# Optimization experiments

Hardware: AMD Instinct MI355X
Metric: run time of the kernel (lower is better)

## Reference

```python
import jax, jax.numpy as jnp
import numpy as np

F_DIM = 128
EDGE_DIM = 41
N_CONV = 6
N_GRAPHS = 128
EPS = 1e-5


def _bn(h, g, b, m, v):
    # eval-mode BatchNorm1d with running stats
    return (h - m) * (g / jnp.sqrt(v + EPS)) + b


def setup_inputs() -> dict:
    key = jax.random.key(0)
    ks = jax.random.split(key, 40)
    N, E = 20000, 320000
    inp = {}
    inp['x'] = jax.random.normal(ks[0], (N, 98), dtype=jnp.float32)
    inp['edge_index'] = jax.random.randint(ks[1], (2, E), 0, N, dtype=jnp.int32)
    inp['edge_attr'] = jax.random.uniform(ks[2], (E, EDGE_DIM), dtype=jnp.float32)
    inp['batch'] = jnp.sort(jax.random.randint(ks[3], (N,), 0, N_GRAPHS, dtype=jnp.int32))
    s = 0.05
    inp['embed_W'] = jax.random.normal(ks[4], (98, F_DIM), dtype=jnp.float32) * s
    inp['embed_b'] = jnp.zeros((F_DIM,), jnp.float32)
    Z = 2 * F_DIM + EDGE_DIM  # 297
    inp['conv_Wf'] = jax.random.normal(ks[5], (N_CONV, Z, F_DIM), dtype=jnp.float32) * s
    inp['conv_bf'] = jnp.zeros((N_CONV, F_DIM), jnp.float32)
    inp['conv_Ws'] = jax.random.normal(ks[6], (N_CONV, Z, F_DIM), dtype=jnp.float32) * s
    inp['conv_bs'] = jnp.zeros((N_CONV, F_DIM), jnp.float32)
    # inner (CGConv) BN params + running stats
    inp['bn_in_g'] = jnp.ones((N_CONV, F_DIM), jnp.float32)
    inp['bn_in_b'] = jnp.zeros((N_CONV, F_DIM), jnp.float32)
    inp['bn_in_m'] = jax.random.normal(ks[7], (N_CONV, F_DIM), dtype=jnp.float32) * 0.1
    inp['bn_in_v'] = jax.random.uniform(ks[8], (N_CONV, F_DIM), dtype=jnp.float32) + 0.5
    # outer BN params + running stats
    inp['bn_out_g'] = jnp.ones((N_CONV, F_DIM), jnp.float32)
    inp['bn_out_b'] = jnp.zeros((N_CONV, F_DIM), jnp.float32)
    inp['bn_out_m'] = jax.random.normal(ks[9], (N_CONV, F_DIM), dtype=jnp.float32) * 0.1
    inp['bn_out_v'] = jax.random.uniform(ks[10], (N_CONV, F_DIM), dtype=jnp.float32) + 0.5
    inp['pool_W'] = jax.random.normal(ks[11], (2 * F_DIM, F_DIM), dtype=jnp.float32) * s
    inp['pool_b'] = jnp.zeros((F_DIM,), jnp.float32)
    inp['f1_W'] = jax.random.normal(ks[12], (F_DIM, 256), dtype=jnp.float32) * s
    inp['f1_b'] = jnp.zeros((256,), jnp.float32)
    inp['f2_W'] = jax.random.normal(ks[13], (256, 128), dtype=jnp.float32) * s
    inp['f2_b'] = jnp.zeros((128,), jnp.float32)
    inp['f3_W'] = jax.random.normal(ks[14], (128, 1), dtype=jnp.float32) * s
    inp['f3_b'] = jnp.zeros((1,), jnp.float32)
    inp['d1_W'] = jax.random.normal(ks[15], (F_DIM, 256), dtype=jnp.float32) * s
    inp['d1_b'] = jnp.zeros((256,), jnp.float32)
    inp['d2_W'] = jax.random.normal(ks[16], (256, 384), dtype=jnp.float32) * s
    inp['d2_b'] = jnp.zeros((384,), jnp.float32)
    return inp


def reference(x, edge_index, edge_attr, batch,
              embed_W, embed_b,
              conv_Wf, conv_bf, conv_Ws, conv_bs,
              bn_in_g, bn_in_b, bn_in_m, bn_in_v,
              bn_out_g, bn_out_b, bn_out_m, bn_out_v,
              pool_W, pool_b,
              f1_W, f1_b, f2_W, f2_b, f3_W, f3_b,
              d1_W, d1_b, d2_W, d2_b):
    N = x.shape[0]
    src, dst = edge_index[0], edge_index[1]  # PyG: messages flow src(j) -> dst(i)
    h = x @ embed_W + embed_b  # [N, F]
    for i in range(N_CONV):
        h_res = h
        # CGConv: z = [x_i, x_j, e_ij]; m = sigmoid(lin_f(z)) * softplus(lin_s(z))
        z = jnp.concatenate([h[dst], h[src], edge_attr], axis=-1)  # [E, 297]
        m = jax.nn.sigmoid(z @ conv_Wf[i] + conv_bf[i]) * jax.nn.softplus(z @ conv_Ws[i] + conv_bs[i])
        agg = jax.ops.segment_sum(m, dst, num_segments=N)  # scatter-add to target nodes
        agg = _bn(agg, bn_in_g[i], bn_in_b[i], bn_in_m[i], bn_in_v[i])  # CGConv internal BN
        h = agg + h  # CGConv residual
        h = _bn(h, bn_out_g[i], bn_out_b[i], bn_out_m[i], bn_out_v[i])  # outer BN
        if i > 0:
            h = h + h_res
        # dropout: identity in eval mode
    # global mean / max pool by graph id
    sums = jax.ops.segment_sum(h, batch, num_segments=N_GRAPHS)
    counts = jax.ops.segment_sum(jnp.ones((N,), h.dtype), batch, num_segments=N_GRAPHS)
    x_mean = sums / jnp.maximum(counts, 1.0)[:, None]
    x_max = jax.ops.segment_max(h, batch, num_segments=N_GRAPHS)
    x_max = jnp.where(jnp.isfinite(x_max), x_max, 0.0)
    x_pool = jnp.concatenate([x_mean, x_max], axis=-1)  # [B, 2F]
    emb = jax.nn.relu(x_pool @ pool_W + pool_b)  # [B, F]
    f = jax.nn.silu(emb @ f1_W + f1_b)
    f = jax.nn.silu(f @ f2_W + f2_b)
    formation = f @ f3_W + f3_b  # [B, 1]
    d = jax.nn.silu(emb @ d1_W + d1_b)
    dos = (d @ d2_W + d2_b).reshape(-1, 3, 128)  # [B, 3, 128]
    return formation, dos
```

## Files before the change

kernel.cpp:

```cpp
#include <hip/hip_runtime.h>
#include <hip/hip_bf16.h>
#include <math.h>

typedef __attribute__((ext_vector_type(8))) _Float16 half8;
typedef __attribute__((ext_vector_type(4))) _Float16 half4;
typedef __attribute__((ext_vector_type(4))) float f32x4;
typedef __attribute__((ext_vector_type(4))) unsigned int u32x4;

#define FDIM 128
#define EPSBN 1e-5f
#define HSCALE_INV 0.015625f
#define WSCALE 64.0f
#define LOG2E 1.4426950408889634f
#define LN2   0.6931471805599453f

__global__ void prep_wn2(const float* __restrict__ Wf, const float* __restrict__ Ws,
                         _Float16* __restrict__ Wn2) {
    int idx = blockIdx.x * 256 + threadIdx.x;
    const int total = 6 * 65536;
    if (idx >= total) return;
    int j = idx & 7;
    int l15 = (idx >> 3) & 15;
    int lhi = (idx >> 7) & 3;
    int cb = (idx >> 9) & 31;
    int c4 = (idx >> 14) & 3;
    int i = idx >> 16;
    int col512 = cb * 16 + l15;
    int which = col512 >> 8;
    int colc = col512 & 255;
    int p = (colc >> 4) & 1;
    int f = ((colc >> 5) << 4) | (colc & 15);
    int k = c4 * 32 + lhi * 8 + j;
    int row = which * 128 + k;
    size_t o = ((size_t)i * 297 + row) * 128 + f;
    Wn2[idx] = (_Float16)((p ? Ws[o] : Wf[o]) * (WSCALE * LOG2E));
}

__global__ void prep_wb2(const float* __restrict__ Wf, const float* __restrict__ Ws,
                         _Float16* __restrict__ Wb2) {
    int idx = blockIdx.x * 256 + threadIdx.x;
    const int total = 6 * 16384;
    if (idx >= total) return;
    int j = idx & 7;
    int l15 = (idx >> 3) & 15;
    int lhi = (idx >> 7) & 3;
    int cb = (idx >> 9) & 15;
    int c2 = (idx >> 13) & 1;
    int i = idx >> 14;
    int k = c2 * 32 + lhi * 8 + j;
    int colc = cb * 16 + l15;
    int p = (colc >> 4) & 1;
    int f = ((colc >> 5) << 4) | (colc & 15);
    float v = 0.0f;
    if (k < 41) {
        size_t o = ((size_t)i * 297 + 256 + k) * 128 + f;
        v = (p ? Ws[o] : Wf[o]) * LOG2E;
    }
    Wb2[idx] = (_Float16)v;
}

__global__ void prep_we(const float* __restrict__ embW, _Float16* __restrict__ We) {
    int idx = blockIdx.x * 256 + threadIdx.x;
    if (idx >= 16384) return;
    int j = idx & 7;
    int l15 = (idx >> 3) & 15;
    int lhi = (idx >> 7) & 3;
    int cb = (idx >> 9) & 7;
    int c4 = (idx >> 12) & 3;
    int k = c4 * 32 + lhi * 8 + j;
    int f = cb * 16 + l15;
    We[idx] = (_Float16)((k < 98) ? embW[k * 128 + f] : 0.0f);
}

__global__ void prep_ht(const float* __restrict__ pW, const float* __restrict__ f1W,
                        const float* __restrict__ f2W, const float* __restrict__ d1W,
                        const float* __restrict__ d2W, float* __restrict__ HT) {
    int idx = blockIdx.x * 256 + threadIdx.x;
    if (idx < 32768) {
        int o = idx >> 8, k = idx & 255;
        HT[o * 256 + k] = pW[k * 128 + o];
    } else if (idx < 65536) {
        int r = idx - 32768; int o = r >> 7, k = r & 127;
        HT[32768 + o * 128 + k] = f1W[k * 256 + o];
    } else if (idx < 98304) {
        int r = idx - 65536; int o = r >> 8, k = r & 255;
        HT[65536 + o * 256 + k] = f2W[k * 128 + o];
    } else if (idx < 131072) {
        int r = idx - 98304; int o = r >> 7, k = r & 127;
        HT[98304 + o * 128 + k] = d1W[k * 256 + o];
    } else if (idx < 229376) {
        int r = idx - 131072; int o = r >> 8, k = r & 255;
        HT[131072 + o * 256 + k] = d2W[k * 384 + o];
    }
}

__global__ void prep_bn(const float* __restrict__ bing, const float* __restrict__ binb,
                        const float* __restrict__ binm, const float* __restrict__ binv,
                        const float* __restrict__ bog, const float* __restrict__ bob,
                        const float* __restrict__ bom, const float* __restrict__ bov,
                        float* __restrict__ ABC) {
    int idx = blockIdx.x * 128 + threadIdx.x;
    if (idx >= 6 * 128) return;
    int f = idx & 127;
    int i = idx >> 7;
    int o = i * 128 + f;
    float gin_ = bing[o] / sqrtf(binv[o] + EPSBN);
    float gout_ = bog[o] / sqrtf(bov[o] + EPSBN);
    ABC[i * 384 + f] = gin_ * gout_ * LN2;
    ABC[i * 384 + 128 + f] = gout_ + ((i > 0) ? 1.0f : 0.0f);
    ABC[i * 384 + 256 + f] = (binb[o] - binm[o] * gin_ - bom[o]) * gout_ + bob[o];
}

__global__ void hist_k(const int* __restrict__ dstI, int* __restrict__ cnt, int E) {
    int e = blockIdx.x * 256 + threadIdx.x;
    if (e < E) atomicAdd(&cnt[dstI[e]], 1);
}

__global__ void scan_k(const int* __restrict__ cnt, int* __restrict__ cursor, int N) {
    __shared__ int part[256];
    int t = threadIdx.x;
    int chunk = (N + 255) / 256;
    int lo = t * chunk, hi = lo + chunk; if (hi > N) hi = N;
    int s = 0;
    for (int i = lo; i < hi; ++i) s += cnt[i];
    part[t] = s;
    __syncthreads();
    for (int d = 1; d < 256; d <<= 1) {
        int v = (t >= d) ? part[t - d] : 0;
        __syncthreads();
        part[t] += v;
        __syncthreads();
    }
    int run = (t > 0) ? part[t - 1] : 0;
    for (int i = lo; i < hi; ++i) { cursor[i] = run; run += cnt[i]; }
}

__global__ void scatter_k(const int* __restrict__ srcI, const int* __restrict__ dstI,
                          int* __restrict__ cursor, unsigned* __restrict__ sdS,
                          int* __restrict__ invE, int E) {
    int e = blockIdx.x * 256 + threadIdx.x;
    if (e >= E) return;
    int d = dstI[e];
    int pos = atomicAdd(&cursor[d], 1);
    sdS[pos] = (unsigned)srcI[e] | ((unsigned)d << 16);
    invE[e] = pos;
}

__global__ void permute_ea2(const float* __restrict__ ea, const int* __restrict__ invE,
                            _Float16* __restrict__ eaH, int E) {
    int e = blockIdx.x * 4 + (threadIdx.x >> 6);
    int c = threadIdx.x & 63;
    if (e >= E) return;
    float v = (c < 41) ? ea[(size_t)e * 41 + c] : 0.0f;
    int pos = invE[e];
    eaH[(size_t)pos * 64 + c] = (_Float16)v;
}

__global__ __launch_bounds__(256, 4)
void embed_mm(const float* __restrict__ x, const _Float16* __restrict__ We,
              const float* __restrict__ b, float* __restrict__ h, int N) {
    __shared__ __align__(16) _Float16 xt[32 * 128];
    const int tid = threadIdx.x;
    const int nb = blockIdx.x * 32;

    {
        int e = tid >> 3, t = tid & 7;
        int node = nb + e; if (node >= N) node = N - 1;
        const float* row = x + (size_t)node * 98;
        __align__(16) _Float16 tmp[16];
        #pragma unroll
        for (int u = 0; u < 16; ++u) {
            int c = t * 16 + u;
            tmp[u] = (c < 98) ? (_Float16)row[c] : (_Float16)0.f;
        }
        int swz = (e & 7) << 4;
        *(u32x4*)((char*)xt + e * 256 + (((2 * t) * 16) ^ swz)) = *(u32x4*)tmp;
        *(u32x4*)((char*)xt + e * 256 + (((2 * t + 1) * 16) ^ swz)) = *(u32x4*)(tmp + 8);
    }
    __syncthreads();

    const int wid = tid >> 6;
    const int lane = tid & 63;
    const int l15 = lane & 15;
    const int lhi = lane >> 4;
    const int swzA = (l15 & 7) << 4;

    f32x4 acc[2][2];
    #pragma unroll
    for (int m = 0; m < 2; ++m)
        #pragma unroll
        for (int n = 0; n < 2; ++n) acc[m][n] = (f32x4){0.f, 0.f, 0.f, 0.f};

    #pragma unroll
    for (int c4 = 0; c4 < 4; ++c4) {
        half8 a[2];
        #pragma unroll
        for (int m = 0; m < 2; ++m) {
            int r = m * 16 + l15;
            a[m] = *(const half8*)((const char*)xt + r * 256 + ((c4 * 64 + lhi * 16) ^ swzA));
        }
        #pragma unroll
        for (int n = 0; n < 2; ++n) {
            int cb = wid * 2 + n;
            const half8 bf = *(const half8*)(We + ((((size_t)c4 * 8 + cb) * 4 + lhi) * 16 + l15) * 8);
            #pragma unroll
            for (int m = 0; m < 2; ++m)
                acc[m][n] = __builtin_amdgcn_mfma_f32_16x16x32_f16(a[m], bf, acc[m][n], 0, 0, 0);
        }
    }

    #pragma unroll
    for (int m = 0; m < 2; ++m) {
        #pragma unroll
        for (int n = 0; n < 2; ++n) {
            int feat = wid * 32 + n * 16 + l15;
            float bias = b[feat];
            #pragma unroll
            for (int j = 0; j < 4; ++j) {
                int node = nb + m * 16 + lhi * 4 + j;
                if (node < N) h[(size_t)node * 128 + feat] = acc[m][n][j] + bias;
            }
        }
    }
}

__global__ __launch_bounds__(256, 4)
void node_gemm_f(float* __restrict__ h, float* __restrict__ agg,
                 const _Float16* __restrict__ WnL, const float* __restrict__ ABC,
                 float* __restrict__ Pd4, float* __restrict__ Ps4, int N, int doBN) {
    __shared__ __align__(16) _Float16 ht[32 * 128];
    const int tid = threadIdx.x;
    const int nb = blockIdx.x * 32;

    {
        int e = tid >> 3, t = tid & 7;
        int node = nb + e; bool ok = (node < N); if (!ok) node = N - 1;
        const int c0 = t * 16;
        float* hrow = h + (size_t)node * 128 + c0;
        __align__(16) _Float16 tmp[16];
        if (doBN && ok) {
            float* arow = agg + (size_t)node * 128 + c0;
            #pragma unroll
            for (int u = 0; u < 16; u += 4) {
                f32x4 av = *(const f32x4*)(arow + u);
                f32x4 hv = *(const f32x4*)(hrow + u);
                f32x4 Av = *(const f32x4*)(ABC + c0 + u);
                f32x4 Bv = *(const f32x4*)(ABC + 128 + c0 + u);
                f32x4 Cv = *(const f32x4*)(ABC + 256 + c0 + u);
                f32x4 xv;
                #pragma unroll
                for (int j = 0; j < 4; ++j)
                    xv[j] = fmaf(av[j], Av[j], fmaf(hv[j], Bv[j], Cv[j]));
                *(f32x4*)(hrow + u) = xv;
                *(f32x4*)(arow + u) = (f32x4){0.f, 0.f, 0.f, 0.f};
                #pragma unroll
                for (int j = 0; j < 4; ++j) tmp[u + j] = (_Float16)(xv[j] * HSCALE_INV);
            }
        } else {
            #pragma unroll
            for (int u = 0; u < 16; u += 4) {
                f32x4 hv = *(const f32x4*)(hrow + u);
                #pragma unroll
                for (int j = 0; j < 4; ++j) tmp[u + j] = (_Float16)(hv[j] * HSCALE_INV);
            }
        }
        int swz = (e & 7) << 4;
        *(u32x4*)((char*)ht + e * 256 + (((2 * t) * 16) ^ swz)) = *(u32x4*)tmp;
        *(u32x4*)((char*)ht + e * 256 + (((2 * t + 1) * 16) ^ swz)) = *(u32x4*)(tmp + 8);
    }
    __syncthreads();

    f32x4 acc[2][8];
    #pragma unroll
    for (int m = 0; m < 2; ++m)
        #pragma unroll
        for (int n = 0; n < 8; ++n) acc[m][n] = (f32x4){0.f, 0.f, 0.f, 0.f};

    const int wid = tid >> 6;
    const int lane = tid & 63;
    const int l15 = lane & 15;
    const int lhi = lane >> 4;
    const int swzA = (l15 & 7) << 4;

    #pragma unroll
    for (int c4 = 0; c4 < 4; ++c4) {
        half8 a[2];
        #pragma unroll
        for (int m = 0; m < 2; ++m) {
            int r = m * 16 + l15;
            a[m] = *(const half8*)((const char*)ht + r * 256 + ((c4 * 64 + lhi * 16) ^ swzA));
        }
        #pragma unroll
        for (int n = 0; n < 8; ++n) {
            int cb = wid * 8 + n;
            const half8 bf = *(const half8*)(WnL +
                             ((((size_t)c4 * 32 + cb) * 4 + lhi) * 16 + l15) * 8);
            #pragma unroll
            for (int m = 0; m < 2; ++m)
                acc[m][n] = __builtin_amdgcn_mfma_f32_16x16x32_f16(a[m], bf, acc[m][n], 0, 0, 0);
        }
    }

    float* base = (wid < 2) ? Pd4 : Ps4;
    const int gw = (wid & 1) * 2;
    #pragma unroll
    for (int m = 0; m < 2; ++m) {
        #pragma unroll
        for (int j = 0; j < 4; ++j) {
            int node = nb + m * 16 + lhi * 4 + j;
            if (node < N) {
                #pragma unroll
                for (int nn = 0; nn < 2; ++nn) {
                    f32x4 v = { acc[m][4 * nn + 0][j], acc[m][4 * nn + 1][j],
                                acc[m][4 * nn + 2][j], acc[m][4 * nn + 3][j] };
                    *(f32x4*)(base + (size_t)node * 256 + ((gw + nn) * 16 + l15) * 4) = v;
                }
            }
        }
    }
}

__global__ __launch_bounds__(256, 4)
void edge_v11(const _Float16* __restrict__ eaH,
              const unsigned* __restrict__ sdS,
              const _Float16* __restrict__ WbL,
              const float* __restrict__ Pd4, const float* __restrict__ Ps4,
              const float* __restrict__ biasF, const float* __restrict__ biasS,
              float* __restrict__ agg) {
    __shared__ __align__(16) _Float16 eacc[64 * 256];
    __shared__ int srcl[64], dstl[64];

    const int tid = threadIdx.x;
    const int nblk = (int)gridDim.x;
    int lb = blockIdx.x;
    if ((nblk & 7) == 0) {
        int q = nblk >> 3;
        lb = (lb & 7) * q + (lb >> 3);
    }
    const int eb = lb * 64;

    if (tid < 64) {
        unsigned sd = sdS[eb + tid];
        srcl[tid] = (int)(sd & 0xFFFFu);
        dstl[tid] = (int)(sd >> 16);
    }

    const int wid = tid >> 6;
    const int lane = tid & 63;
    const int l15 = lane & 15;
    const int lhi = lane >> 4;

    f32x4 acc[4][4];
    #pragma unroll
    for (int m = 0; m < 4; ++m)
        #pragma unroll
        for (int n = 0; n < 4; ++n) acc[m][n] = (f32x4){0.f, 0.f, 0.f, 0.f};

    #pragma unroll
    for (int c2 = 0; c2 < 2; ++c2) {
        half8 a[4];
        #pragma unroll
        for (int m = 0; m < 4; ++m) {
            int r = m * 16 + l15;
            a[m] = *(const half8*)(eaH + (size_t)(eb + r) * 64 + c2 * 32 + lhi * 8);
        }
        #pragma unroll
        for (int n = 0; n < 4; ++n) {
            int cb = wid * 4 + n;
            const half8 b = *(const half8*)(WbL +
                            ((((size_t)c2 * 16 + cb) * 4 + lhi) * 16 + l15) * 8);
            #pragma unroll
            for (int m = 0; m < 4; ++m)
                acc[m][n] = __builtin_amdgcn_mfma_f32_16x16x32_f16(a[m], b, acc[m][n], 0, 0, 0);
        }
    }

    {
        const int g = (wid << 4) | l15;
        #pragma unroll
        for (int m = 0; m < 4; ++m) {
            #pragma unroll
            for (int j = 0; j < 4; ++j) {
                int r = m * 16 + lhi * 4 + j;
                half4 hv;
                hv[0] = (_Float16)acc[m][0][j];
                hv[1] = (_Float16)acc[m][1][j];
                hv[2] = (_Float16)acc[m][2][j];
                hv[3] = (_Float16)acc[m][3][j];
                *(half4*)(eacc + r * 256 + g * 4) = hv;
            }
        }
    }
    __syncthreads();

    const int f0 = ((lane >> 4) << 5) | l15;
    f32x4 b4;
    b4[0] = biasF[f0] * LOG2E;
    b4[1] = biasS[f0] * LOG2E;
    b4[2] = biasF[f0 + 16] * LOG2E;
    b4[3] = biasS[f0 + 16] * LOG2E;
    const int rbase = wid * 16;

    float s0 = 0.f, s1 = 0.f;
    int prevd = dstl[rbase];
    f32x4 pdb = *(const f32x4*)(Pd4 + (size_t)prevd * 256 + lane * 4);
    pdb += b4;

    f32x4 psq[4];
    #pragma unroll
    for (int e = 0; e < 4; ++e)
        psq[e] = *(const f32x4*)(Ps4 + (size_t)srcl[rbase + e] * 256 + lane * 4);

    #pragma unroll
    for (int e = 0; e < 16; ++e) {
        int r = rbase + e;
        int d = dstl[r];
        if (d != prevd) {
            pdb = *(const f32x4*)(Pd4 + (size_t)d * 256 + lane * 4);
            pdb += b4;
            prevd = d;
        }
        f32x4 psv = psq[e & 3];
        if (e + 4 < 16)
            psq[e & 3] = *(const f32x4*)(Ps4 + (size_t)srcl[r + 4] * 256 + lane * 4);
        half4 ev = *(const half4*)(eacc + r * 256 + lane * 4);
        float fp0 = (float)ev[0] + pdb[0] + psv[0];
        float sp0 = (float)ev[1] + pdb[1] + psv[1];
        float fp1 = (float)ev[2] + pdb[2] + psv[2];
        float sp1 = (float)ev[3] + pdb[3] + psv[3];
        float sig0 = __builtin_amdgcn_rcpf(1.0f + exp2f(-fp0));
        float spl0 = fmaxf(sp0, 0.0f) + __log2f(1.0f + exp2f(-fabsf(sp0)));
        float sig1 = __builtin_amdgcn_rcpf(1.0f + exp2f(-fp1));
        float spl1 = fmaxf(sp1, 0.0f) + __log2f(1.0f + exp2f(-fabsf(sp1)));
        s0 += sig0 * spl0;
        s1 += sig1 * spl1;
        bool flush = (e == 15) || (dstl[r + 1] != d);
        if (flush) {
            atomicAdd(&agg[(size_t)d * 128 + f0], s0);
            atomicAdd(&agg[(size_t)d * 128 + f0 + 16], s1);
            s0 = 0.f; s1 = 0.f;
        }
    }
}

__global__ void bn_final(const float* __restrict__ agg, float* __restrict__ h,
                         const float* __restrict__ ABC, int n128) {
    int idx = blockIdx.x * 256 + threadIdx.x;
    if (idx >= n128) return;
    int f = idx & 127;
    h[idx] = fmaf(agg[idx], ABC[f], fmaf(h[idx], ABC[128 + f], ABC[256 + f]));
}

__global__ __launch_bounds__(256, 4)
void pool2_k(const float* __restrict__ h, const int* __restrict__ batch,
             float* __restrict__ sums, unsigned* __restrict__ maxs,
             float* __restrict__ counts, int N) {
    const int f = threadIdx.x & 127;
    const int half = threadIdx.x >> 7;
    const int nb = blockIdx.x * 64 + half * 32;
    if (nb >= N) return;

    float s = 0.f;
    float mx = -3.4e38f;
    int prevg = -1;
    int runlen = 0;

    for (int e = 0; e < 32; ++e) {
        int n = nb + e;
        if (n >= N) break;
        int g = batch[n];
        if (g != prevg) {
            if (prevg >= 0) {
                atomicAdd(&sums[prevg * 128 + f], s);
                unsigned u = __float_as_uint(mx);
                unsigned key = (u & 0x80000000u) ? ~u : (u | 0x80000000u);
                atomicMax(&maxs[prevg * 128 + f], key);
                if (f == 0) atomicAdd(&counts[prevg], (float)runlen);
            }
            s = 0.f; mx = -3.4e38f; runlen = 0; prevg = g;
        }
        float v = h[(size_t)n * 128 + f];
        s += v;
        mx = fmaxf(mx, v);
        ++runlen;
    }
    if (prevg >= 0) {
        atomicAdd(&sums[prevg * 128 + f], s);
        unsigned u = __float_as_uint(mx);
        unsigned key = (u & 0x80000000u) ? ~u : (u | 0x80000000u);
        atomicMax(&maxs[prevg * 128 + f], key);
        if (f == 0) atomicAdd(&counts[prevg], (float)runlen);
    }
}

__global__ __launch_bounds__(256)
void head_k2(const float* __restrict__ sums, const unsigned* __restrict__ maxs,
             const float* __restrict__ counts, const float* __restrict__ HT,
             const float* __restrict__ pb, const float* __restrict__ f1b,
             const float* __restrict__ f2b, const float* __restrict__ f3W,
             const float* __restrict__ f3b, const float* __restrict__ d1b,
             const float* __restrict__ d2b, float* __restrict__ out) {
    __shared__ float xp[256], emb[128], s1[256], s2[128], dd[256];
    int g = blockIdx.x, t = threadIdx.x;
    float cnt = counts[g];
    if (t < 128) {
        float mean = sums[g * 128 + t] / fmaxf(cnt, 1.0f);
        float mx = 0.0f;
        if (cnt > 0.0f) {
            unsigned key = maxs[g * 128 + t];
            unsigned u = (key & 0x80000000u) ? (key & 0x7fffffffu) : ~key;
            mx = __uint_as_float(u);
            if (!isfinite(mx)) mx = 0.0f;
        }
        xp[t] = mean;
        xp[128 + t] = mx;
    }
    __syncthreads();
    if (t < 128) {
        const float* w = HT + t * 256;
        float a0 = 0.f, a1 = 0.f, a2 = 0.f, a3 = 0.f;
        #pragma unroll
        for (int k = 0; k < 256; k += 4) {
            f32x4 wv = *(const f32x4*)(w + k);
            a0 = fmaf(xp[k + 0], wv[0], a0);
            a1 = fmaf(xp[k + 1], wv[1], a1);
            a2 = fmaf(xp[k + 2], wv[2], a2);
            a3 = fmaf(xp[k + 3], wv[3], a3);
        }
        emb[t] = fmaxf((a0 + a1) + (a2 + a3) + pb[t], 0.0f);
    }
    __syncthreads();
    {
        const float* w = HT + 32768 + t * 128;
        float a0 = 0.f, a1 = 0.f, a2 = 0.f, a3 = 0.f;
        #pragma unroll
        for (int k = 0; k < 128; k += 4) {
            f32x4 wv = *(const f32x4*)(w + k);
            a0 = fmaf(emb[k + 0], wv[0], a0);
            a1 = fmaf(emb[k + 1], wv[1], a1);
            a2 = fmaf(emb[k + 2], wv[2], a2);
            a3 = fmaf(emb[k + 3], wv[3], a3);
        }
        float a = (a0 + a1) + (a2 + a3) + f1b[t];
        s1[t] = a / (1.0f + __expf(-a));
    }
    __syncthreads();
    if (t < 128) {
        const float* w = HT + 65536 + t * 256;
        float a0 = 0.f, a1 = 0.f, a2 = 0.f, a3 = 0.f;
        #pragma unroll
        for (int k = 0; k < 256; k += 4) {
            f32x4 wv = *(const f32x4*)(w + k);
            a0 = fmaf(s1[k + 0], wv[0], a0);
            a1 = fmaf(s1[k + 1], wv[1], a1);
            a2 = fmaf(s1[k + 2], wv[2], a2);
            a3 = fmaf(s1[k + 3], wv[3], a3);
        }
        float a = (a0 + a1) + (a2 + a3) + f2b[t];
        s2[t] = a / (1.0f + __expf(-a));
    }
    {
        const float* w = HT + 98304 + t * 128;
        float a0 = 0.f, a1 = 0.f, a2 = 0.f, a3 = 0.f;
        #pragma unroll
        for (int k = 0; k < 128; k += 4) {
            f32x4 wv = *(const f32x4*)(w + k);
            a0 = fmaf(emb[k + 0], wv[0], a0);
            a1 = fmaf(emb[k + 1], wv[1], a1);
            a2 = fmaf(emb[k + 2], wv[2], a2);
            a3 = fmaf(emb[k + 3], wv[3], a3);
        }
        float a = (a0 + a1) + (a2 + a3) + d1b[t];
        dd[t] = a / (1.0f + __expf(-a));
    }
    __syncthreads();
    if (t == 0) {
        float a = f3b[0];
        for (int k = 0; k < 128; ++k) a = fmaf(s2[k], f3W[k], a);
        out[g] = a;
    }
    #pragma unroll
    for (int o = t; o < 384; o += 256) {
        const float* w = HT + 131072 + o * 256;
        float a0 = 0.f, a1 = 0.f, a2 = 0.f, a3 = 0.f;
        #pragma unroll
        for (int k = 0; k < 256; k += 4) {
            f32x4 wv = *(const f32x4*)(w + k);
            a0 = fmaf(dd[k + 0], wv[0], a0);
            a1 = fmaf(dd[k + 1], wv[1], a1);
            a2 = fmaf(dd[k + 2], wv[2], a2);
            a3 = fmaf(dd[k + 3], wv[3], a3);
        }
        out[128 + (size_t)g * 384 + o] = (a0 + a1) + (a2 + a3) + d2b[o];
    }
}

extern "C" void kernel_launch(void* const* d_in, const int* in_sizes, int n_in,
                              void* d_out, int out_size, void* d_ws, size_t ws_size,
                              hipStream_t stream) {
    const float* x       = (const float*)d_in[0];
    const int*   eidx    = (const int*)d_in[1];
    const float* ea      = (const float*)d_in[2];
    const int*   batch   = (const int*)d_in[3];
    const float* embW    = (const float*)d_in[4];
    const float* embB    = (const float*)d_in[5];
    const float* convWf  = (const float*)d_in[6];
    const float* convbf  = (const float*)d_in[7];
    const float* convWs  = (const float*)d_in[8];
    const float* convbs  = (const float*)d_in[9];
    const float* bing    = (const float*)d_in[10];
    const float* binb    = (const float*)d_in[11];
    const float* binm    = (const float*)d_in[12];
    const float* binv    = (const float*)d_in[13];
    const float* bog     = (const float*)d_in[14];
    const float* bob     = (const float*)d_in[15];
    const float* bom     = (const float*)d_in[16];
    const float* bov     = (const float*)d_in[17];
    const float* pW      = (const float*)d_in[18];
    const float* pb      = (const float*)d_in[19];
    const float* f1W     = (const float*)d_in[20];
    const float* f1b     = (const float*)d_in[21];
    const float* f2W     = (const float*)d_in[22];
    const float* f2b     = (const float*)d_in[23];
    const float* f3W     = (const float*)d_in[24];
    const float* f3b     = (const float*)d_in[25];
    const float* d1W     = (const float*)d_in[26];
    const float* d1b     = (const float*)d_in[27];
    const float* d2W     = (const float*)d_in[28];
    const float* d2b     = (const float*)d_in[29];

    const int N = in_sizes[0] / 98;
    const int E = in_sizes[1] / 2;
    const int* srcI = eidx;
    const int* dstI = eidx + E;

    char* ws = (char*)d_ws;
    float* h        = (float*)(ws);
    float* agg      = (float*)(ws + 10240000);
    float* Pd4      = (float*)(ws + 20480000);
    float* Ps4      = (float*)(ws + 40960000);
    _Float16* Wn2   = (_Float16*)(ws + 61440000);
    _Float16* Wb2   = (_Float16*)(ws + 62226432);
    float* sums     = (float*)(ws + 62423040);
    unsigned* maxs  = (unsigned*)(ws + 62488576);
    float* gcnt     = (float*)(ws + 62554112);
    unsigned* sdS   = (unsigned*)(ws + 62554624);
    int* invE       = (int*)(ws + 63834624);
    _Float16* eaH   = (_Float16*)(ws + 65114624);
    float* ABC      = (float*)(ws + 106074624);
    _Float16* We    = (_Float16*)(ws + 106083840);
    float* HT       = (float*)(ws + 106116608);
    int* nodeCnt    = (int*)(ws + 20480000);
    int* cursor     = nodeCnt + N;

    prep_wn2<<<(6 * 65536) / 256, 256, 0, stream>>>(convWf, convWs, Wn2);
    prep_wb2<<<(6 * 16384 + 255) / 256, 256, 0, stream>>>(convWf, convWs, Wb2);
    prep_we<<<64, 256, 0, stream>>>(embW, We);
    prep_ht<<<(229376 + 255) / 256, 256, 0, stream>>>(pW, f1W, f2W, d1W, d2W, HT);
    prep_bn<<<6, 128, 0, stream>>>(bing, binb, binm, binv, bog, bob, bom, bov, ABC);
    hipMemsetAsync(nodeCnt, 0, (size_t)N * 4, stream);
    hist_k<<<(E + 255) / 256, 256, 0, stream>>>(dstI, nodeCnt, E);
    scan_k<<<1, 256, 0, stream>>>(nodeCnt, cursor, N);
    scatter_k<<<(E + 255) / 256, 256, 0, stream>>>(srcI, dstI, cursor, sdS, invE, E);
    permute_ea2<<<(E + 3) / 4, 256, 0, stream>>>(ea, invE, eaH, E);

    const int n128 = N * 128;
    const int nblk = (N + 31) / 32;
    embed_mm<<<nblk, 256, 0, stream>>>(x, We, embB, h, N);

    hipMemsetAsync(agg, 0, (size_t)n128 * 4, stream);
    for (int i = 0; i < 6; ++i) {
        node_gemm_f<<<nblk, 256, 0, stream>>>(h, agg, Wn2 + (size_t)i * 65536,
                                              ABC + (size_t)(i - 1) * 384,
                                              Pd4, Ps4, N, (i > 0) ? 1 : 0);
        edge_v11<<<E / 64, 256, 0, stream>>>(eaH, sdS,
                                             Wb2 + (size_t)i * 16384,
                                             Pd4, Ps4, convbf + i * 128, convbs + i * 128, agg);
    }
    bn_final<<<(n128 + 255) / 256, 256, 0, stream>>>(agg, h, ABC + 5 * 384, n128);

    hipMemsetAsync(sums, 0, 65536 + 65536 + 512, stream);
    pool2_k<<<(N + 63) / 64, 256, 0, stream>>>(h, batch, sums, maxs, gcnt, N);
    head_k2<<<128, 256, 0, stream>>>(sums, maxs, gcnt, HT, pb, f1b, f2b, f3W, f3b,
                                     d1b, d2b, (float*)d_out);
}
```

Before: 640.8 us.

## Halve edge kernel LDS staging for higher occupancy and fuse final BN into pooling

The edge kernel now stages the fp16 edge pre-activations through shared memory in two 32-row halves instead of one 64-row buffer. This halves LDS per block, and the launch-bounds occupancy hint is raised from 4 to 6 blocks. Each wave now handles 8 rows per half, at the cost of an extra barrier and shorter per-dst accumulation runs, which can mean more atomics. The standalone final BN kernel is removed and its affine transform is applied inside the pooling kernel, saving one full pass over the node features.

After: 914.0 us. 42.6% more time.

```diff
diff --git a/kernel.cpp b/kernel.cpp
--- a/kernel.cpp
+++ b/kernel.cpp
@@ -320,14 +320,14 @@
     }
 }
 
-__global__ __launch_bounds__(256, 4)
-void edge_v11(const _Float16* __restrict__ eaH,
+__global__ __launch_bounds__(256, 6)
+void edge_v12(const _Float16* __restrict__ eaH,
               const unsigned* __restrict__ sdS,
               const _Float16* __restrict__ WbL,
               const float* __restrict__ Pd4, const float* __restrict__ Ps4,
               const float* __restrict__ biasF, const float* __restrict__ biasS,
               float* __restrict__ agg) {
-    __shared__ __align__(16) _Float16 eacc[64 * 256];
+    __shared__ __align__(16) _Float16 eacc[32 * 256];
     __shared__ int srcl[64], dstl[64];
 
     const int tid = threadIdx.x;
@@ -375,84 +375,88 @@
         }
     }
 
-    {
-        const int g = (wid << 4) | l15;
-        #pragma unroll
-        for (int m = 0; m < 4; ++m) {
-            #pragma unroll
-            for (int j = 0; j < 4; ++j) {
-                int r = m * 16 + lhi * 4 + j;
-                half4 hv;
-                hv[0] = (_Float16)acc[m][0][j];
-                hv[1] = (_Float16)acc[m][1][j];
-                hv[2] = (_Float16)acc[m][2][j];
-                hv[3] = (_Float16)acc[m][3][j];
-                *(half4*)(eacc + r * 256 + g * 4) = hv;
-            }
-        }
-    }
-    __syncthreads();
-
+    const int g = (wid << 4) | l15;
     const int f0 = ((lane >> 4) << 5) | l15;
     f32x4 b4;
     b4[0] = biasF[f0] * LOG2E;
     b4[1] = biasS[f0] * LOG2E;
     b4[2] = biasF[f0 + 16] * LOG2E;
     b4[3] = biasS[f0 + 16] * LOG2E;
-    const int rbase = wid * 16;
-
-    float s0 = 0.f, s1 = 0.f;
-    int prevd = dstl[rbase];
-    f32x4 pdb = *(const f32x4*)(Pd4 + (size_t)prevd * 256 + lane * 4);
-    pdb += b4;
-
-    f32x4 psq[4];
-    #pragma unroll
-    for (int e = 0; e < 4; ++e)
-        psq[e] = *(const f32x4*)(Ps4 + (size_t)srcl[rbase + e] * 256 + lane * 4);
-
-    #pragma unroll
-    for (int e = 0; e < 16; ++e) {
-        int r = rbase + e;
-        int d = dstl[r];
-        if (d != prevd) {
-            pdb = *(const f32x4*)(Pd4 + (size_t)d * 256 + lane * 4);
-            pdb += b4;
-            prevd = d;
-        }
-        f32x4 psv = psq[e & 3];
-        if (e + 4 < 16)
-            psq[e & 3] = *(const f32x4*)(Ps4 + (size_t)srcl[r + 4] * 256 + lane * 4);
-        half4 ev = *(const half4*)(eacc + r * 256 + lane * 4);
-        float fp0 = (float)ev[0] + pdb[0] + psv[0];
-        float sp0 = (float)ev[1] + pdb[1] + psv[1];
-        float fp1 = (float)ev[2] + pdb[2] + psv[2];
-        float sp1 = (float)ev[3] + pdb[3] + psv[3];
-        float sig0 = __builtin_amdgcn_rcpf(1.0f + exp2f(-fp0));
-        float spl0 = fmaxf(sp0, 0.0f) + __log2f(1.0f + exp2f(-fabsf(sp0)));
-        float sig1 = __builtin_amdgcn_rcpf(1.0f + exp2f(-fp1));
-        float spl1 = fmaxf(sp1, 0.0f) + __log2f(1.0f + exp2f(-fabsf(sp1)));
-        s0 += sig0 * spl0;
-        s1 += sig1 * spl1;
-        bool flush = (e == 15) || (dstl[r + 1] != d);
-        if (flush) {
-            atomicAdd(&agg[(size_t)d * 128 + f0], s0);
-            atomicAdd(&agg[(size_t)d * 128 + f0 + 16], s1);
-            s0 = 0.f; s1 = 0.f;
-        }
-    }
-}
-
-__global__ void bn_final(const float* __restrict__ agg, float* __restrict__ h,
-                         const float* __restrict__ ABC, int n128) {
-    int idx = blockIdx.x * 256 + threadIdx.x;
-    if (idx >= n128) return;
-    int f = idx & 127;
-    h[idx] = fmaf(agg[idx], ABC[f], fmaf(h[idx], ABC[128 + f], ABC[256 + f]));
+
+    int prevd = -1;
+    f32x4 pdb;
+
+    #pragma unroll
+    for (int half = 0; half < 2; ++half) {
+        #pragma unroll
+        for (int mm = 0; mm < 2; ++mm) {
+            int m = half * 2 + mm;
+            #pragma unroll
+            for (int j = 0; j < 4; ++j) {
+                int lr = mm * 16 + lhi * 4 + j;
+                half4 hv;
+                hv[0] = (_Float16)acc[m][0][j];
+                hv[1] = (_Float16)acc[m][1][j];
+                hv[2] = (_Float16)acc[m][2][j];
+                hv[3] = (_Float16)acc[m][3][j];
+                *(half4*)(eacc + lr * 256 + g * 4) = hv;
+            }
+        }
+        __syncthreads();
+
+        const int rbase = half * 32 + wid * 8;
+        float s0 = 0.f, s1 = 0.f;
+        {
+            int d0 = dstl[rbase];
+            if (d0 != prevd) {
+                pdb = *(const f32x4*)(Pd4 + (size_t)d0 * 256 + lane * 4);
+                pdb += b4;
+                prevd = d0;
+            }
+        }
+        f32x4 psq[4];
+        #pragma unroll
+        for (int e = 0; e < 4; ++e)
+            psq[e] = *(const f32x4*)(Ps4 + (size_t)srcl[rbase + e] * 256 + lane * 4);
+
+        #pragma unroll
+        for (int e = 0; e < 8; ++e) {
+            int r = rbase + e;
+            int d = dstl[r];
+            if (d != prevd) {
+                pdb = *(const f32x4*)(Pd4 + (size_t)d * 256 + lane * 4);
+                pdb += b4;
+                prevd = d;
+            }
+            f32x4 psv = psq[e & 3];
+            if (e + 4 < 8)
+                psq[e & 3] = *(const f32x4*)(Ps4 + (size_t)srcl[r + 4] * 256 + lane * 4);
+            int lr = r - half * 32;
+            half4 ev = *(const half4*)(eacc + lr * 256 + lane * 4);
+            float fp0 = (float)ev[0] + pdb[0] + psv[0];
+            float sp0 = (float)ev[1] + pdb[1] + psv[1];
+            float fp1 = (float)ev[2] + pdb[2] + psv[2];
+            float sp1 = (float)ev[3] + pdb[3] + psv[3];
+            float sig0 = __builtin_amdgcn_rcpf(1.0f + exp2f(-fp0));
+            float spl0 = fmaxf(sp0, 0.0f) + __log2f(1.0f + exp2f(-fabsf(sp0)));
+            float sig1 = __builtin_amdgcn_rcpf(1.0f + exp2f(-fp1));
+            float spl1 = fmaxf(sp1, 0.0f) + __log2f(1.0f + exp2f(-fabsf(sp1)));
+            s0 += sig0 * spl0;
+            s1 += sig1 * spl1;
+            bool flush = (e == 7) || (dstl[r + 1] != d);
+            if (flush) {
+                atomicAdd(&agg[(size_t)d * 128 + f0], s0);
+                atomicAdd(&agg[(size_t)d * 128 + f0 + 16], s1);
+                s0 = 0.f; s1 = 0.f;
+            }
+        }
+        if (half == 0) __syncthreads();
+    }
 }
 
 __global__ __launch_bounds__(256, 4)
-void pool2_k(const float* __restrict__ h, const int* __restrict__ batch,
+void pool3_k(const float* __restrict__ agg, const float* __restrict__ h,
+             const float* __restrict__ ABC5, const int* __restrict__ batch,
              float* __restrict__ sums, unsigned* __restrict__ maxs,
              float* __restrict__ counts, int N) {
     const int f = threadIdx.x & 127;
@@ -460,6 +464,7 @@
     const int nb = blockIdx.x * 64 + half * 32;
     if (nb >= N) return;
 
+    const float A = ABC5[f], B = ABC5[128 + f], C = ABC5[256 + f];
     float s = 0.f;
     float mx = -3.4e38f;
     int prevg = -1;
@@ -479,7 +484,7 @@
             }
             s = 0.f; mx = -3.4e38f; runlen = 0; prevg = g;
         }
-        float v = h[(size_t)n * 128 + f];
+        float v = fmaf(agg[(size_t)n * 128 + f], A, fmaf(h[(size_t)n * 128 + f], B, C));
         s += v;
         mx = fmaxf(mx, v);
         ++runlen;
@@ -673,14 +678,14 @@
         node_gemm_f<<<nblk, 256, 0, stream>>>(h, agg, Wn2 + (size_t)i * 65536,
                                               ABC + (size_t)(i - 1) * 384,
                                               Pd4, Ps4, N, (i > 0) ? 1 : 0);
-        edge_v11<<<E / 64, 256, 0, stream>>>(eaH, sdS,
+        edge_v12<<<E / 64, 256, 0, stream>>>(eaH, sdS,
                                              Wb2 + (size_t)i * 16384,
                                              Pd4, Ps4, convbf + i * 128, convbs + i * 128, agg);
     }
-    bn_final<<<(n128 + 255) / 256, 256, 0, stream>>>(agg, h, ABC + 5 * 384, n128);
 
     hipMemsetAsync(sums, 0, 65536 + 65536 + 512, stream);
-    pool2_k<<<(N + 63) / 64, 256, 0, stream>>>(h, batch, sums, maxs, gcnt, N);
+    pool3_k<<<(N + 63) / 64, 256, 0, stream>>>(agg, h, ABC + 5 * 384, batch,
+                                               sums, maxs, gcnt, N);
     head_k2<<<128, 256, 0, stream>>>(sums, maxs, gcnt, HT, pb, f1b, f2b, f3W, f3b,
                                      d1b, d2b, (float*)d_out);
 }
```
